# Optimization experiments

Measured on AMD Instinct MI355X. Metric: run time of the kernel, lower is better.

The kernel has to match this reference:

```python
import jax, jax.numpy as jnp
import numpy as np
from jax import lax

ALPHA = 0.3  # SSGConv alpha


def _cdist(x):
    # Euclidean distance matrix [N, N] for x: [N, H]
    n2 = jnp.sum(x * x, axis=-1)
    d2 = n2[:, None] + n2[None, :] - 2.0 * (x @ x.T)
    return jnp.sqrt(jnp.maximum(d2, 0.0))


def _prim(dist):
    # Dense O(N^2) Prim MST starting at node 0. Returns (parents, children, weights), each [N-1].
    N = dist.shape[0]
    INF = jnp.float32(1e30)
    in_tree = jnp.zeros(N, dtype=bool).at[0].set(True)
    mind = dist[0]                       # best edge weight into tree per node
    parent = jnp.zeros(N, dtype=jnp.int32)

    def step(carry, _):
        in_tree, mind, parent = carry
        d = jnp.where(in_tree, INF, mind)
        v = jnp.argmin(d).astype(jnp.int32)
        w = d[v]
        p = parent[v]
        in_tree = in_tree.at[v].set(True)
        newd = dist[v]
        upd = newd < mind
        mind = jnp.where(upd, newd, mind)
        parent = jnp.where(upd, v, parent)
        return (in_tree, mind, parent), (p, v, w)

    _, (ps, vs, ws) = lax.scan(step, (in_tree, mind, parent), None, length=N - 1)
    return ps, vs, ws


def _build_edges(features):
    # Torch code detaches edge weights via .item(); mirror with stop_gradient.
    B, N, _ = features.shape
    dist = jax.vmap(_cdist)(lax.stop_gradient(features))   # [B, N, N]
    ps, vs, ws = jax.vmap(_prim)(dist)                     # each [B, N-1]
    off = (jnp.arange(B, dtype=jnp.int32) * N)[:, None]
    a = (ps + off).ravel()
    b = (vs + off).ravel()
    src = jnp.concatenate([a, b])   # MST edges are added in both directions
    dst = jnp.concatenate([b, a])
    ew = jnp.concatenate([ws.ravel(), ws.ravel()])
    return src, dst, ew


def _gcn_norm(src, dst, ew, num_nodes):
    # PyG gcn_norm: add self loops (weight 1), symmetric deg^-1/2 normalization.
    loop = jnp.arange(num_nodes, dtype=src.dtype)
    src = jnp.concatenate([src, loop])
    dst = jnp.concatenate([dst, loop])
    ew = jnp.concatenate([ew, jnp.ones(num_nodes, ew.dtype)])
    deg = jax.ops.segment_sum(ew, dst, num_segments=num_nodes)
    dinv = jnp.where(deg > 0, lax.rsqrt(jnp.maximum(deg, 1e-30)), 0.0)
    norm = dinv[src] * ew * dinv[dst]
    return src, dst, norm


def _ssg_conv(x, src, dst, norm, W, b, num_nodes):
    # SSGConv with K=1: h = alpha*x + (1-alpha)*A_hat x, then linear.
    prop = jax.ops.segment_sum(norm[:, None] * x[src], dst, num_segments=num_nodes)
    h = ALPHA * x + (1.0 - ALPHA) * prop
    return h @ W + b


def _forward(features, W1, b1, W2, b2, W3, b3, Wd, bd, Wo, bo):
    B, N, H = features.shape
    NT = B * N
    src, dst, ew = _build_edges(features)
    src, dst, norm = _gcn_norm(src, dst, ew, NT)
    x = features.reshape(NT, H)
    x = jnp.tanh(_ssg_conv(x, src, dst, norm, W1, b1, NT))
    x = jnp.tanh(_ssg_conv(x, src, dst, norm, W2, b2, NT))
    x = jnp.tanh(_ssg_conv(x, src, dst, norm, W3, b3, NT))
    # dropout: eval mode -> identity. global_mean_pool: each graph has exactly N nodes.
    pooled = x.reshape(B, N, -1).mean(axis=1)          # [B, 2H]
    h = jnp.tanh(pooled @ Wd + bd)                     # [B, H]
    return h @ Wo + bo                                 # [B, num_labels]


def setup_inputs() -> dict:
    key = jax.random.key(0)
    ks = jax.random.split(key, 12)
    B, N, H, L = 16, 1024, 256, 8
    H2 = 2 * H

    def lin(k, fin, fout):
        s = 1.0 / np.sqrt(fin)
        k1, k2 = jax.random.split(k)
        return (jax.random.uniform(k1, (fin, fout), jnp.float32, -s, s),
                jax.random.uniform(k2, (fout,), jnp.float32, -s, s))

    W1, b1 = lin(ks[1], H, H2)
    W2, b2 = lin(ks[2], H2, H2)
    W3, b3 = lin(ks[3], H2, H2)
    Wd, bd = lin(ks[4], H2, H)
    Wo, bo = lin(ks[5], H, L)
    features = jax.random.normal(ks[0], (B, N, H), jnp.float32)
    return {"features": features, "W1": W1, "b1": b1, "W2": W2, "b2": b2,
            "W3": W3, "b3": b3, "Wd": Wd, "bd": bd, "Wo": Wo, "bo": bo}


def reference(features, W1, b1, W2, b2, W3, b3, Wd, bd, Wo, bo):
    return _forward(features, W1, b1, W2, b2, W3, b3, Wd, bd, Wo, bo)
```

## Files before the change

kernel.cpp:

```cpp
#include <hip/hip_runtime.h>
#include <math.h>

namespace {

constexpr float ALPHA = 0.3f;
constexpr int B  = 16;
constexpr int N  = 1024;
constexpr int H  = 256;
constexpr int H2 = 512;
constexpr int NT = B * N;
constexpr int NE = N - 1;
constexpr int CAP = 32;

__device__ __forceinline__ unsigned umin32(unsigned a, unsigned b) { return a < b ? a : b; }

__global__ void n2_kernel(const float* __restrict__ x, float* __restrict__ n2) {
  int wave = threadIdx.x >> 6, lane = threadIdx.x & 63;
  int row  = blockIdx.x * 4 + wave;
  float4 v = *(const float4*)(x + (size_t)row * H + lane * 4);
  float s  = v.x * v.x + v.y * v.y + v.z * v.z + v.w * v.w;
  #pragma unroll
  for (int off = 32; off; off >>= 1) s += __shfl_xor(s, off);
  if (lane == 0) n2[row] = s;
}

__global__ __launch_bounds__(256) void dist_kernel(const float* __restrict__ x,
    const float* __restrict__ n2, float* __restrict__ dist) {
  __shared__ float As[16][132], Bs[16][132];
  const int bb = blockIdx.z;
  const int i0 = blockIdx.y * 128, j0 = blockIdx.x * 128;
  const int t = threadIdx.x, tx = t & 15, ty = t >> 4;
  const float* xb = x + (size_t)bb * N * H;
  float acc[8][8] = {};
  for (int kc = 0; kc < H; kc += 16) {
    #pragma unroll
    for (int u = 0; u < 2; ++u) {
      int q = t + u * 256;
      int row = q >> 2, kf = (q & 3) * 4;
      float4 a = *(const float4*)(xb + (size_t)(i0 + row) * H + kc + kf);
      As[kf + 0][row] = a.x; As[kf + 1][row] = a.y;
      As[kf + 2][row] = a.z; As[kf + 3][row] = a.w;
      float4 bv = *(const float4*)(xb + (size_t)(j0 + row) * H + kc + kf);
      Bs[kf + 0][row] = bv.x; Bs[kf + 1][row] = bv.y;
      Bs[kf + 2][row] = bv.z; Bs[kf + 3][row] = bv.w;
    }
    __syncthreads();
    #pragma unroll
    for (int kk = 0; kk < 16; ++kk) {
      float4 a0 = *(const float4*)&As[kk][ty * 4];
      float4 a1 = *(const float4*)&As[kk][64 + ty * 4];
      float4 b0 = *(const float4*)&Bs[kk][tx * 4];
      float4 b1 = *(const float4*)&Bs[kk][64 + tx * 4];
      float ar[8] = {a0.x,a0.y,a0.z,a0.w,a1.x,a1.y,a1.z,a1.w};
      float br[8] = {b0.x,b0.y,b0.z,b0.w,b1.x,b1.y,b1.z,b1.w};
      #pragma unroll
      for (int r = 0; r < 8; ++r)
        #pragma unroll
        for (int c = 0; c < 8; ++c) acc[r][c] += ar[r] * br[c];
    }
    __syncthreads();
  }
  float n2i[8], n2j[8];
  #pragma unroll
  for (int r = 0; r < 8; ++r)
    n2i[r] = n2[bb * N + i0 + (r < 4 ? ty * 4 + r : 64 + ty * 4 + r - 4)];
  #pragma unroll
  for (int c = 0; c < 8; ++c)
    n2j[c] = n2[bb * N + j0 + (c < 4 ? tx * 4 + c : 64 + tx * 4 + c - 4)];
  #pragma unroll
  for (int r = 0; r < 8; ++r) {
    int mi = i0 + (r < 4 ? ty * 4 + r : 64 + ty * 4 + r - 4);
    float o[8];
    #pragma unroll
    for (int c = 0; c < 8; ++c) {
      float d2 = (n2i[r] + n2j[c]) - 2.0f * acc[r][c];
      o[c] = sqrtf(fmaxf(d2, 0.0f));
    }
    float* dst = dist + ((size_t)bb * N + mi) * N + j0;
    *(float4*)(dst + tx * 4)      = make_float4(o[0], o[1], o[2], o[3]);
    *(float4*)(dst + 64 + tx * 4) = make_float4(o[4], o[5], o[6], o[7]);
  }
}

__device__ __forceinline__ unsigned wave_min_u32(unsigned x) {
  unsigned t;
  t = (unsigned)__builtin_amdgcn_update_dpp((int)x, (int)x, 0x111, 0xf, 0xf, false); x = umin32(x, t);
  t = (unsigned)__builtin_amdgcn_update_dpp((int)x, (int)x, 0x112, 0xf, 0xf, false); x = umin32(x, t);
  t = (unsigned)__builtin_amdgcn_update_dpp((int)x, (int)x, 0x114, 0xf, 0xf, false); x = umin32(x, t);
  t = (unsigned)__builtin_amdgcn_update_dpp((int)x, (int)x, 0x118, 0xf, 0xf, false); x = umin32(x, t);
  x = umin32(x, (unsigned)__shfl_xor((int)x, 16));
  x = umin32(x, (unsigned)__shfl_xor((int)x, 32));
  return (unsigned)__builtin_amdgcn_readlane((int)x, 63);
}

struct Sel2 { unsigned w; int j; };

__device__ __forceinline__ Sel2 block_select(unsigned mw0, unsigned mw1,
    unsigned mw2, unsigned mw3, int wid, int lane, unsigned long long* smin) {
  unsigned lm = umin32(umin32(mw0, mw1), umin32(mw2, mw3));
  unsigned wm = wave_min_u32(lm);
  unsigned mb = (mw0 == wm ? 1u : 0u) | (mw1 == wm ? 2u : 0u) |
                (mw2 == wm ? 4u : 0u) | (mw3 == wm ? 8u : 0u);
  unsigned long long bal = __ballot(mb != 0);
  int fl = __ffsll(bal) - 1;
  int slot = __ffs((unsigned)__builtin_amdgcn_readlane((int)mb, fl)) - 1;
  int widx = (wid << 8) | (fl << 2) | slot;
  if (lane == 0)
    smin[wid] = ((unsigned long long)wm << 32) | (unsigned)widx;
  __syncthreads();
  unsigned long long k0 = smin[0], k1 = smin[1], k2 = smin[2], k3 = smin[3];
  unsigned long long ka = k0 < k1 ? k0 : k1;
  unsigned long long kb = k2 < k3 ? k2 : k3;
  unsigned long long kk = ka < kb ? ka : kb;
  __syncthreads();
  Sel2 r; r.w = (unsigned)(kk >> 32); r.j = (int)(unsigned)(kk & 0xFFFFFFFFu);
  return r;
}

__global__ __launch_bounds__(256, 1) void prim_kernel(const float* __restrict__ dist,
    int* __restrict__ ep, int* __restrict__ ev, float* __restrict__ ewt) {
  __shared__ unsigned long long smin[4];
  __shared__ int epv[NE];
  __shared__ int evv[NE];
  __shared__ float ews[NE];
  const int b = blockIdx.x;
  const int tid = threadIdx.x, wid = tid >> 6, lane = tid & 63;
  const float* Db = dist + (size_t)b * N * N;
  const int jbase = tid * 4;

  unsigned d0, d1, d2, d3;
  {
    float4 v = *(const float4*)(Db + jbase);
    d0 = __float_as_uint(v.x); d1 = __float_as_uint(v.y);
    d2 = __float_as_uint(v.z); d3 = __float_as_uint(v.w);
  }
  unsigned mw0 = d0, mw1 = d1, mw2 = d2, mw3 = d3;
  unsigned rm0 = 0, rm1 = 0, rm2 = 0, rm3 = 0;
  int pa0 = 0, pa1 = 0, pa2 = 0, pa3 = 0;
  if (tid == 0) { rm0 = ~0u; mw0 = ~0u; }

  Sel2 s0 = block_select(mw0, mw1, mw2, mw3, wid, lane, smin);
  int cj = s0.j;
  if ((cj >> 2) == tid) {
    int sl = cj & 3;
    int pv = pa0; if (sl == 1) pv = pa1; if (sl == 2) pv = pa2; if (sl == 3) pv = pa3;
    epv[0] = pv; evv[0] = cj; ews[0] = __uint_as_float(s0.w);
    if (sl == 0) { rm0 = ~0u; mw0 = ~0u; }
    if (sl == 1) { rm1 = ~0u; mw1 = ~0u; }
    if (sl == 2) { rm2 = ~0u; mw2 = ~0u; }
    if (sl == 3) { rm3 = ~0u; mw3 = ~0u; }
  }
  float4 xq = *(const float4*)(Db + (size_t)cj * N + jbase);

  for (int k = 1; k < NE; ++k) {
    unsigned r0 = __float_as_uint(xq.x), r1 = __float_as_uint(xq.y);
    unsigned r2 = __float_as_uint(xq.z), r3 = __float_as_uint(xq.w);
    unsigned q0 = r0 | rm0, q1 = r1 | rm1, q2 = r2 | rm2, q3 = r3 | rm3;
    mw0 = umin32(mw0, q0); mw1 = umin32(mw1, q1);
    mw2 = umin32(mw2, q2); mw3 = umin32(mw3, q3);
    Sel2 se = block_select(mw0, mw1, mw2, mw3, wid, lane, smin);
    const int nj = se.j;
    float4 nxt = *(const float4*)(Db + (size_t)nj * N + jbase);
    if (r0 < d0) { pa0 = cj; d0 = r0; }
    if (r1 < d1) { pa1 = cj; d1 = r1; }
    if (r2 < d2) { pa2 = cj; d2 = r2; }
    if (r3 < d3) { pa3 = cj; d3 = r3; }
    if ((nj >> 2) == tid) {
      int sl = nj & 3;
      int pv = pa0; if (sl == 1) pv = pa1; if (sl == 2) pv = pa2; if (sl == 3) pv = pa3;
      epv[k] = pv; evv[k] = nj; ews[k] = __uint_as_float(se.w);
      if (sl == 0) { rm0 = ~0u; mw0 = ~0u; }
      if (sl == 1) { rm1 = ~0u; mw1 = ~0u; }
      if (sl == 2) { rm2 = ~0u; mw2 = ~0u; }
      if (sl == 3) { rm3 = ~0u; mw3 = ~0u; }
    }
    cj = nj; xq = nxt;
  }

  __syncthreads();
  for (int e = tid; e < NE; e += 256) {
    ep[b * NE + e]  = epv[e];
    ev[b * NE + e]  = evv[e];
    ewt[b * NE + e] = ews[e];
  }
}

__global__ void adj_kernel(const int* __restrict__ ep, const int* __restrict__ ev,
    const float* __restrict__ ewt, int* __restrict__ adjI, float* __restrict__ adjW,
    int* __restrict__ cnt, float* __restrict__ dinv) {
  int i = blockIdx.x * 256 + threadIdx.x;
  int b = i >> 10, loc = i & 1023;
  const int* epb = ep + b * NE;
  const int* evb = ev + b * NE;
  const float* ewb = ewt + b * NE;
  int c = 0; float wsum = 0.0f;
  for (int k = 0; k < NE; ++k) {
    int p = epb[k], v = evb[k];
    if (p == loc || v == loc) {
      float w = ewb[k];
      wsum += w;
      int nb = (p == loc) ? v : p;
      if (c < CAP) { adjI[i * CAP + c] = (b << 10) + nb; adjW[i * CAP + c] = w; }
      ++c;
    }
  }
  cnt[i]  = c < CAP ? c : CAP;
  dinv[i] = 1.0f / sqrtf(wsum + 1.0f);
}

template <int HH>
__global__ void prop_kernel(const float* __restrict__ x, const int* __restrict__ adjI,
    const float* __restrict__ adjW, const int* __restrict__ cnt,
    const float* __restrict__ dinv, float* __restrict__ h) {
  constexpr int U = HH / 256;
  int wave = threadIdx.x >> 6, lane = threadIdx.x & 63;
  int i = blockIdx.x * 4 + wave;
  float dv = dinv[i];
  int c = cnt[i];
  float selfc = ALPHA + (1.0f - ALPHA) * dv * dv;
  float4 acc[U];
  const float* xi = x + (size_t)i * HH + lane * 4;
  #pragma unroll
  for (int u = 0; u < U; ++u) {
    float4 v = *(const float4*)(xi + u * 256);
    acc[u].x = selfc * v.x; acc[u].y = selfc * v.y;
    acc[u].z = selfc * v.z; acc[u].w = selfc * v.w;
  }
  for (int e = 0; e < c; ++e) {
    int j   = adjI[i * CAP + e];
    float w = adjW[i * CAP + e];
    float coef = (1.0f - ALPHA) * dv * (w * dinv[j]);
    const float* xj = x + (size_t)j * HH + lane * 4;
    #pragma unroll
    for (int u = 0; u < U; ++u) {
      float4 v = *(const float4*)(xj + u * 256);
      acc[u].x += coef * v.x; acc[u].y += coef * v.y;
      acc[u].z += coef * v.z; acc[u].w += coef * v.w;
    }
  }
  float* ho = h + (size_t)i * HH + lane * 4;
  #pragma unroll
  for (int u = 0; u < U; ++u) *(float4*)(ho + u * 256) = acc[u];
}

template <int K>
__global__ __launch_bounds__(256) void gemm_tanh_kernel(const float* __restrict__ A,
    const float* __restrict__ W, const float* __restrict__ bias, float* __restrict__ C) {
  __shared__ float As[16][132], Bs[16][132];
  const int m0 = blockIdx.x * 128, n0 = blockIdx.y * 128;
  const int t = threadIdx.x, tx = t & 15, ty = t >> 4;
  float acc[8][8] = {};
  for (int kc = 0; kc < K; kc += 16) {
    #pragma unroll
    for (int u = 0; u < 2; ++u) {
      int q = t + u * 256;
      int row = q >> 2, kf = (q & 3) * 4;
      float4 a = *(const float4*)(A + (size_t)(m0 + row) * K + kc + kf);
      As[kf + 0][row] = a.x; As[kf + 1][row] = a.y;
      As[kf + 2][row] = a.z; As[kf + 3][row] = a.w;
      int rowB = q >> 5, cf = (q & 31) * 4;
      *(float4*)&Bs[rowB][cf] = *(const float4*)(W + (size_t)(kc + rowB) * H2 + n0 + cf);
    }
    __syncthreads();
    #pragma unroll
    for (int kk = 0; kk < 16; ++kk) {
      float4 a0 = *(const float4*)&As[kk][ty * 4];
      float4 a1 = *(const float4*)&As[kk][64 + ty * 4];
      float4 b0 = *(const float4*)&Bs[kk][tx * 4];
      float4 b1 = *(const float4*)&Bs[kk][64 + tx * 4];
      float ar[8] = {a0.x,a0.y,a0.z,a0.w,a1.x,a1.y,a1.z,a1.w};
      float br[8] = {b0.x,b0.y,b0.z,b0.w,b1.x,b1.y,b1.z,b1.w};
      #pragma unroll
      for (int r = 0; r < 8; ++r)
        #pragma unroll
        for (int c = 0; c < 8; ++c) acc[r][c] += ar[r] * br[c];
    }
    __syncthreads();
  }
  float4 bi0 = *(const float4*)(bias + n0 + tx * 4);
  float4 bi1 = *(const float4*)(bias + n0 + 64 + tx * 4);
  float bb[8] = {bi0.x,bi0.y,bi0.z,bi0.w,bi1.x,bi1.y,bi1.z,bi1.w};
  #pragma unroll
  for (int r = 0; r < 8; ++r) {
    int m = m0 + (r < 4 ? ty * 4 + r : 64 + ty * 4 + r - 4);
    float o[8];
    #pragma unroll
    for (int c = 0; c < 8; ++c) o[c] = tanhf(acc[r][c] + bb[c]);
    float* dst = C + (size_t)m * H2 + n0;
    *(float4*)(dst + tx * 4)      = make_float4(o[0], o[1], o[2], o[3]);
    *(float4*)(dst + 64 + tx * 4) = make_float4(o[4], o[5], o[6], o[7]);
  }
}

__global__ void pool_kernel(const float* __restrict__ x, float* __restrict__ pooled) {
  int b = blockIdx.x;
  int c = blockIdx.y * 256 + threadIdx.x;
  const float* xb = x + ((size_t)b << 10) * H2 + c;
  float s = 0.0f;
  for (int i = 0; i < N; ++i) s += xb[(size_t)i * H2];
  pooled[b * H2 + c] = s * (1.0f / N);
}

__global__ void head_kernel(const float* __restrict__ pooled, const float* __restrict__ Wd,
    const float* __restrict__ bd, const float* __restrict__ Wo, const float* __restrict__ bo,
    float* __restrict__ out) {
  __shared__ float sp[512], sh[256];
  int b = blockIdx.x, t = threadIdx.x;
  sp[t] = pooled[b * H2 + t];
  sp[t + 256] = pooled[b * H2 + t + 256];
  __syncthreads();
  float acc = bd[t];
  for (int c2 = 0; c2 < 512; ++c2) acc += sp[c2] * Wd[c2 * 256 + t];
  sh[t] = tanhf(acc);
  __syncthreads();
  if (t < 8) {
    float o = bo[t];
    for (int j = 0; j < 256; ++j) o += sh[j] * Wo[j * 8 + t];
    out[b * 8 + t] = o;
  }
}

}

extern "C" void kernel_launch(void* const* d_in, const int* in_sizes, int n_in,
                              void* d_out, int out_size, void* d_ws, size_t ws_size,
                              hipStream_t stream) {
  const float* feat = (const float*)d_in[0];
  const float* W1 = (const float*)d_in[1];
  const float* b1 = (const float*)d_in[2];
  const float* W2 = (const float*)d_in[3];
  const float* b2 = (const float*)d_in[4];
  const float* W3 = (const float*)d_in[5];
  const float* b3 = (const float*)d_in[6];
  const float* Wd = (const float*)d_in[7];
  const float* bd = (const float*)d_in[8];
  const float* Wo = (const float*)d_in[9];
  const float* bo = (const float*)d_in[10];
  float* out = (float*)d_out;
  char* ws = (char*)d_ws;

  float* dist = (float*)(ws);
  float* xcur = (float*)(ws);
  float* hbuf = (float*)(ws + ((size_t)64 << 20));
  char* misc  = ws + ((size_t)96 << 20);
  int*   ep     = (int*)(misc);
  int*   ev     = (int*)(misc + 65536);
  float* ewt    = (float*)(misc + 131072);
  int*   cnt    = (int*)(misc + 196608);
  float* dinv   = (float*)(misc + 262144);
  int*   adjI   = (int*)(misc + 327680);
  float* adjW   = (float*)(misc + 327680 + 2097152);
  float* n2     = (float*)(misc + 327680 + 2 * 2097152);
  float* pooled = (float*)(misc + 327680 + 2 * 2097152 + 65536);

  n2_kernel<<<NT / 4, 256, 0, stream>>>(feat, n2);
  dist_kernel<<<dim3(8, 8, 16), 256, 0, stream>>>(feat, n2, dist);
  prim_kernel<<<B, 256, 0, stream>>>(dist, ep, ev, ewt);
  adj_kernel<<<NT / 256, 256, 0, stream>>>(ep, ev, ewt, adjI, adjW, cnt, dinv);

  prop_kernel<256><<<NT / 4, 256, 0, stream>>>(feat, adjI, adjW, cnt, dinv, hbuf);
  gemm_tanh_kernel<256><<<dim3(NT / 128, 4), 256, 0, stream>>>(hbuf, W1, b1, xcur);
  prop_kernel<512><<<NT / 4, 256, 0, stream>>>(xcur, adjI, adjW, cnt, dinv, hbuf);
  gemm_tanh_kernel<512><<<dim3(NT / 128, 4), 256, 0, stream>>>(hbuf, W2, b2, xcur);
  prop_kernel<512><<<NT / 4, 256, 0, stream>>>(xcur, adjI, adjW, cnt, dinv, hbuf);
  gemm_tanh_kernel<512><<<dim3(NT / 128, 4), 256, 0, stream>>>(hbuf, W3, b3, xcur);

  pool_kernel<<<dim3(B, H2 / 256), 256, 0, stream>>>(xcur, pooled);
  head_kernel<<<B, 256, 0, stream>>>(pooled, Wd, bd, Wo, bo, out);
}
```

Measured before the change: 1.300 ms.

## Speculatively prefetch runner-up Prim row and drop second barrier via double-buffered shared slots

```diff
diff --git a/kernel.cpp b/kernel.cpp
--- a/kernel.cpp
+++ b/kernel.cpp
@@ -93,10 +93,11 @@
   return (unsigned)__builtin_amdgcn_readlane((int)x, 63);
 }
 
-struct Sel2 { unsigned w; int j; };
-
-__device__ __forceinline__ Sel2 block_select(unsigned mw0, unsigned mw1,
-    unsigned mw2, unsigned mw3, int wid, int lane, unsigned long long* smin) {
+struct Sel3 { unsigned w; int j; int j2; };
+
+__device__ __forceinline__ Sel3 block_select2(unsigned mw0, unsigned mw1,
+    unsigned mw2, unsigned mw3, int tid, int wid, int lane,
+    unsigned long long (*s1)[4], unsigned long long (*s2)[4], int pb) {
   unsigned lm = umin32(umin32(mw0, mw1), umin32(mw2, mw3));
   unsigned wm = wave_min_u32(lm);
   unsigned mb = (mw0 == wm ? 1u : 0u) | (mw1 == wm ? 2u : 0u) |
@@ -104,22 +105,83 @@
   unsigned long long bal = __ballot(mb != 0);
   int fl = __ffsll(bal) - 1;
   int slot = __ffs((unsigned)__builtin_amdgcn_readlane((int)mb, fl)) - 1;
-  int widx = (wid << 8) | (fl << 2) | slot;
-  if (lane == 0)
-    smin[wid] = ((unsigned long long)wm << 32) | (unsigned)widx;
+  int wj = (wid << 8) | (fl << 2) | slot;
+  unsigned e0 = mw0, e1 = mw1, e2 = mw2, e3 = mw3;
+  if (tid == (wj >> 2)) {
+    int sl = wj & 3;
+    if (sl == 0) e0 = ~0u; else if (sl == 1) e1 = ~0u;
+    else if (sl == 2) e2 = ~0u; else e3 = ~0u;
+  }
+  unsigned lm2 = umin32(umin32(e0, e1), umin32(e2, e3));
+  unsigned wm2 = wave_min_u32(lm2);
+  unsigned mb2 = (e0 == wm2 ? 1u : 0u) | (e1 == wm2 ? 2u : 0u) |
+                 (e2 == wm2 ? 4u : 0u) | (e3 == wm2 ? 8u : 0u);
+  unsigned long long bal2 = __ballot(mb2 != 0);
+  int fl2 = __ffsll(bal2) - 1;
+  int slot2 = __ffs((unsigned)__builtin_amdgcn_readlane((int)mb2, fl2)) - 1;
+  int wj2 = (wid << 8) | (fl2 << 2) | slot2;
+  if (lane == 0) {
+    s1[pb][wid] = ((unsigned long long)wm  << 32) | (unsigned)wj;
+    s2[pb][wid] = ((unsigned long long)wm2 << 32) | (unsigned)wj2;
+  }
   __syncthreads();
-  unsigned long long k0 = smin[0], k1 = smin[1], k2 = smin[2], k3 = smin[3];
-  unsigned long long ka = k0 < k1 ? k0 : k1;
-  unsigned long long kb = k2 < k3 ? k2 : k3;
-  unsigned long long kk = ka < kb ? ka : kb;
-  __syncthreads();
-  Sel2 r; r.w = (unsigned)(kk >> 32); r.j = (int)(unsigned)(kk & 0xFFFFFFFFu);
+  unsigned long long a0 = s1[pb][0], a1 = s1[pb][1], a2 = s1[pb][2], a3 = s1[pb][3];
+  unsigned long long b0 = s2[pb][0], b1 = s2[pb][1], b2 = s2[pb][2], b3 = s2[pb][3];
+  unsigned long long w01 = a0 < a1 ? a0 : a1, w23 = a2 < a3 ? a2 : a3;
+  unsigned long long win = w01 < w23 ? w01 : w23;
+  unsigned long long c0 = (a0 == win) ? b0 : a0;
+  unsigned long long c1 = (a1 == win) ? b1 : a1;
+  unsigned long long c2 = (a2 == win) ? b2 : a2;
+  unsigned long long c3 = (a3 == win) ? b3 : a3;
+  unsigned long long r01 = c0 < c1 ? c0 : c1, r23 = c2 < c3 ? c2 : c3;
+  unsigned long long run = r01 < r23 ? r01 : r23;
+  Sel3 r;
+  r.w  = (unsigned)(win >> 32);
+  r.j  = (int)(unsigned)(win & 0x3FFu);
+  r.j2 = (int)(unsigned)(run & 0x3FFu);
   return r;
 }
+
+__device__ __forceinline__ void load16(const float* p, float4& x) {
+  asm volatile("global_load_dwordx4 %0, %1, off" : "=&v"(x) : "v"(p) : "memory");
+}
+
+#define PIN4(V) asm volatile("" :: "v"((V).x), "v"((V).y), "v"((V).z), "v"((V).w))
+
+#define PRIM_ITER(kk, PB, DEAD)                                                   \
+  {                                                                               \
+    asm volatile("s_waitcnt vmcnt(1)" ::: "memory");        \
+    __builtin_amdgcn_sched_barrier(0);                        \
+    PIN4(DEAD);                                       \
+    unsigned r0 = __float_as_uint(xq.x), r1 = __float_as_uint(xq.y);              \
+    unsigned r2 = __float_as_uint(xq.z), r3 = __float_as_uint(xq.w);              \
+    unsigned q0 = r0 | rm0, q1 = r1 | rm1, q2 = r2 | rm2, q3 = r3 | rm3;          \
+    mw0 = umin32(mw0, q0); mw1 = umin32(mw1, q1);                                 \
+    mw2 = umin32(mw2, q2); mw3 = umin32(mw3, q3);                                 \
+    Sel3 se = block_select2(mw0, mw1, mw2, mw3, tid, wid, lane, s1, s2, PB);      \
+    const int nj = se.j;                                                          \
+    load16(Db + (size_t)nj * N + jbase, xq);               \
+    load16(Db + (size_t)se.j2 * N + jbase, DEAD);           \
+    if (r0 < d0) { pa0 = cj; d0 = r0; }                \
+    if (r1 < d1) { pa1 = cj; d1 = r1; }                                           \
+    if (r2 < d2) { pa2 = cj; d2 = r2; }                                           \
+    if (r3 < d3) { pa3 = cj; d3 = r3; }                                           \
+    if ((nj >> 2) == tid) {                               \
+      int sl = nj & 3;                                                            \
+      int pv = pa0; if (sl == 1) pv = pa1; if (sl == 2) pv = pa2;                 \
+      if (sl == 3) pv = pa3;                                                      \
+      epv[kk] = pv; evv[kk] = nj; ews[kk] = __uint_as_float(se.w);                \
+      if (sl == 0) { rm0 = ~0u; mw0 = ~0u; }                                      \
+      if (sl == 1) { rm1 = ~0u; mw1 = ~0u; }                                      \
+      if (sl == 2) { rm2 = ~0u; mw2 = ~0u; }                                      \
+      if (sl == 3) { rm3 = ~0u; mw3 = ~0u; }                                      \
+    }                                                                             \
+    cj = nj;                                                                      \
+  }
 
 __global__ __launch_bounds__(256, 1) void prim_kernel(const float* __restrict__ dist,
     int* __restrict__ ep, int* __restrict__ ev, float* __restrict__ ewt) {
-  __shared__ unsigned long long smin[4];
+  __shared__ unsigned long long s1[2][4], s2[2][4];
   __shared__ int epv[NE];
   __shared__ int evv[NE];
   __shared__ float ews[NE];
@@ -139,7 +201,7 @@
   int pa0 = 0, pa1 = 0, pa2 = 0, pa3 = 0;
   if (tid == 0) { rm0 = ~0u; mw0 = ~0u; }
 
-  Sel2 s0 = block_select(mw0, mw1, mw2, mw3, wid, lane, smin);
+  Sel3 s0 = block_select2(mw0, mw1, mw2, mw3, tid, wid, lane, s1, s2, 0);
   int cj = s0.j;
   if ((cj >> 2) == tid) {
     int sl = cj & 3;
@@ -150,33 +212,19 @@
     if (sl == 2) { rm2 = ~0u; mw2 = ~0u; }
     if (sl == 3) { rm3 = ~0u; mw3 = ~0u; }
   }
-  float4 xq = *(const float4*)(Db + (size_t)cj * N + jbase);
-
-  for (int k = 1; k < NE; ++k) {
-    unsigned r0 = __float_as_uint(xq.x), r1 = __float_as_uint(xq.y);
-    unsigned r2 = __float_as_uint(xq.z), r3 = __float_as_uint(xq.w);
-    unsigned q0 = r0 | rm0, q1 = r1 | rm1, q2 = r2 | rm2, q3 = r3 | rm3;
-    mw0 = umin32(mw0, q0); mw1 = umin32(mw1, q1);
-    mw2 = umin32(mw2, q2); mw3 = umin32(mw3, q3);
-    Sel2 se = block_select(mw0, mw1, mw2, mw3, wid, lane, smin);
-    const int nj = se.j;
-    float4 nxt = *(const float4*)(Db + (size_t)nj * N + jbase);
-    if (r0 < d0) { pa0 = cj; d0 = r0; }
-    if (r1 < d1) { pa1 = cj; d1 = r1; }
-    if (r2 < d2) { pa2 = cj; d2 = r2; }
-    if (r3 < d3) { pa3 = cj; d3 = r3; }
-    if ((nj >> 2) == tid) {
-      int sl = nj & 3;
-      int pv = pa0; if (sl == 1) pv = pa1; if (sl == 2) pv = pa2; if (sl == 3) pv = pa3;
-      epv[k] = pv; evv[k] = nj; ews[k] = __uint_as_float(se.w);
-      if (sl == 0) { rm0 = ~0u; mw0 = ~0u; }
-      if (sl == 1) { rm1 = ~0u; mw1 = ~0u; }
-      if (sl == 2) { rm2 = ~0u; mw2 = ~0u; }
-      if (sl == 3) { rm3 = ~0u; mw3 = ~0u; }
-    }
-    cj = nj; xq = nxt;
-  }
-
+  float4 xq;
+  float4 deadA = make_float4(0.f, 0.f, 0.f, 0.f);
+  float4 deadB = make_float4(0.f, 0.f, 0.f, 0.f);
+  load16(Db + (size_t)cj * N + jbase, xq);
+  load16(Db + (size_t)s0.j2 * N + jbase, deadB);
+
+  for (int k = 1; k + 1 < NE; k += 2) {
+    PRIM_ITER(k,     1, deadA);
+    PRIM_ITER(k + 1, 0, deadB);
+  }
+
+  asm volatile("s_waitcnt vmcnt(0)" ::: "memory");
+  PIN4(deadA); PIN4(deadB); PIN4(xq);
   __syncthreads();
   for (int e = tid; e < NE; e += 256) {
     ep[b * NE + e]  = epv[e];
```

After: 1.623 ms. 24.8% more time.

## Fuse graph propagation into GEMM A-tile loading

Applied to the files above, without the earlier changes.

```diff
diff --git a/kernel.cpp b/kernel.cpp
--- a/kernel.cpp
+++ b/kernel.cpp
@@ -208,56 +208,49 @@
   dinv[i] = 1.0f / sqrtf(wsum + 1.0f);
 }
 
-template <int HH>
-__global__ void prop_kernel(const float* __restrict__ x, const int* __restrict__ adjI,
+template <int K>
+__global__ __launch_bounds__(256) void fgemm_tanh_kernel(
+    const float* __restrict__ x, const int* __restrict__ adjI,
     const float* __restrict__ adjW, const int* __restrict__ cnt,
-    const float* __restrict__ dinv, float* __restrict__ h) {
-  constexpr int U = HH / 256;
-  int wave = threadIdx.x >> 6, lane = threadIdx.x & 63;
-  int i = blockIdx.x * 4 + wave;
-  float dv = dinv[i];
-  int c = cnt[i];
-  float selfc = ALPHA + (1.0f - ALPHA) * dv * dv;
-  float4 acc[U];
-  const float* xi = x + (size_t)i * HH + lane * 4;
-  #pragma unroll
-  for (int u = 0; u < U; ++u) {
-    float4 v = *(const float4*)(xi + u * 256);
-    acc[u].x = selfc * v.x; acc[u].y = selfc * v.y;
-    acc[u].z = selfc * v.z; acc[u].w = selfc * v.w;
-  }
-  for (int e = 0; e < c; ++e) {
-    int j   = adjI[i * CAP + e];
-    float w = adjW[i * CAP + e];
-    float coef = (1.0f - ALPHA) * dv * (w * dinv[j]);
-    const float* xj = x + (size_t)j * HH + lane * 4;
-    #pragma unroll
-    for (int u = 0; u < U; ++u) {
-      float4 v = *(const float4*)(xj + u * 256);
-      acc[u].x += coef * v.x; acc[u].y += coef * v.y;
-      acc[u].z += coef * v.z; acc[u].w += coef * v.w;
-    }
-  }
-  float* ho = h + (size_t)i * HH + lane * 4;
-  #pragma unroll
-  for (int u = 0; u < U; ++u) *(float4*)(ho + u * 256) = acc[u];
-}
-
-template <int K>
-__global__ __launch_bounds__(256) void gemm_tanh_kernel(const float* __restrict__ A,
-    const float* __restrict__ W, const float* __restrict__ bias, float* __restrict__ C) {
+    const float* __restrict__ dinv, const float* __restrict__ W,
+    const float* __restrict__ bias, float* __restrict__ C) {
   __shared__ float As[16][132], Bs[16][132];
   const int m0 = blockIdx.x * 128, n0 = blockIdx.y * 128;
   const int t = threadIdx.x, tx = t & 15, ty = t >> 4;
+  const int row0 = t >> 2, kf0 = (t & 3) * 4;
+  const int row1 = row0 + 64;
+  const int ig0 = m0 + row0, ig1 = m0 + row1;
+  const float dv0 = dinv[ig0], dv1 = dinv[ig1];
+  const int   c0 = cnt[ig0],  c1 = cnt[ig1];
+  const float sf0 = ALPHA + (1.0f - ALPHA) * dv0 * dv0;
+  const float sf1 = ALPHA + (1.0f - ALPHA) * dv1 * dv1;
   float acc[8][8] = {};
   for (int kc = 0; kc < K; kc += 16) {
+    {
+      float4 a = *(const float4*)(x + (size_t)ig0 * K + kc + kf0);
+      float hx = sf0*a.x, hy = sf0*a.y, hz = sf0*a.z, hw = sf0*a.w;
+      for (int e = 0; e < c0; ++e) {
+        int j = adjI[ig0 * CAP + e];
+        float coef = (1.0f - ALPHA) * dv0 * (adjW[ig0 * CAP + e] * dinv[j]);
+        float4 v = *(const float4*)(x + (size_t)j * K + kc + kf0);
+        hx += coef*v.x; hy += coef*v.y; hz += coef*v.z; hw += coef*v.w;
+      }
+      As[kf0+0][row0]=hx; As[kf0+1][row0]=hy; As[kf0+2][row0]=hz; As[kf0+3][row0]=hw;
+    }
+    {
+      float4 a = *(const float4*)(x + (size_t)ig1 * K + kc + kf0);
+      float hx = sf1*a.x, hy = sf1*a.y, hz = sf1*a.z, hw = sf1*a.w;
+      for (int e = 0; e < c1; ++e) {
+        int j = adjI[ig1 * CAP + e];
+        float coef = (1.0f - ALPHA) * dv1 * (adjW[ig1 * CAP + e] * dinv[j]);
+        float4 v = *(const float4*)(x + (size_t)j * K + kc + kf0);
+        hx += coef*v.x; hy += coef*v.y; hz += coef*v.z; hw += coef*v.w;
+      }
+      As[kf0+0][row1]=hx; As[kf0+1][row1]=hy; As[kf0+2][row1]=hz; As[kf0+3][row1]=hw;
+    }
     #pragma unroll
     for (int u = 0; u < 2; ++u) {
       int q = t + u * 256;
-      int row = q >> 2, kf = (q & 3) * 4;
-      float4 a = *(const float4*)(A + (size_t)(m0 + row) * K + kc + kf);
-      As[kf + 0][row] = a.x; As[kf + 1][row] = a.y;
-      As[kf + 2][row] = a.z; As[kf + 3][row] = a.w;
       int rowB = q >> 5, cf = (q & 31) * 4;
       *(float4*)&Bs[rowB][cf] = *(const float4*)(W + (size_t)(kc + rowB) * H2 + n0 + cf);
     }
@@ -340,8 +333,8 @@
   char* ws = (char*)d_ws;
 
   float* dist = (float*)(ws);
-  float* xcur = (float*)(ws);
-  float* hbuf = (float*)(ws + ((size_t)64 << 20));
+  float* buf1 = (float*)(ws);
+  float* buf2 = (float*)(ws + ((size_t)64 << 20));
   char* misc  = ws + ((size_t)96 << 20);
   int*   ep     = (int*)(misc);
   int*   ev     = (int*)(misc + 65536);
@@ -358,13 +351,13 @@
   prim_kernel<<<B, 256, 0, stream>>>(dist, ep, ev, ewt);
   adj_kernel<<<NT / 256, 256, 0, stream>>>(ep, ev, ewt, adjI, adjW, cnt, dinv);
 
-  prop_kernel<256><<<NT / 4, 256, 0, stream>>>(feat, adjI, adjW, cnt, dinv, hbuf);
-  gemm_tanh_kernel<256><<<dim3(NT / 128, 4), 256, 0, stream>>>(hbuf, W1, b1, xcur);
-  prop_kernel<512><<<NT / 4, 256, 0, stream>>>(xcur, adjI, adjW, cnt, dinv, hbuf);
-  gemm_tanh_kernel<512><<<dim3(NT / 128, 4), 256, 0, stream>>>(hbuf, W2, b2, xcur);
-  prop_kernel<512><<<NT / 4, 256, 0, stream>>>(xcur, adjI, adjW, cnt, dinv, hbuf);
-  gemm_tanh_kernel<512><<<dim3(NT / 128, 4), 256, 0, stream>>>(hbuf, W3, b3, xcur);
-
-  pool_kernel<<<dim3(B, H2 / 256), 256, 0, stream>>>(xcur, pooled);
+  fgemm_tanh_kernel<256><<<dim3(NT / 128, 4), 256, 0, stream>>>(
+      feat, adjI, adjW, cnt, dinv, W1, b1, buf1);
+  fgemm_tanh_kernel<512><<<dim3(NT / 128, 4), 256, 0, stream>>>(
+      buf1, adjI, adjW, cnt, dinv, W2, b2, buf2);
+  fgemm_tanh_kernel<512><<<dim3(NT / 128, 4), 256, 0, stream>>>(
+      buf2, adjI, adjW, cnt, dinv, W3, b3, buf1);
+
+  pool_kernel<<<dim3(B, H2 / 256), 256, 0, stream>>>(buf1, pooled);
   head_kernel<<<B, 256, 0, stream>>>(pooled, Wd, bd, Wo, bo, out);
 }
```

Result: slower. 2.510 ms (+93.2%).

## Overlap layer-1 GEMM with Prim MST and exploit distance symmetry

Applied to the files above, without the earlier changes.

```diff
diff --git a/kernel.cpp b/kernel.cpp
--- a/kernel.cpp
+++ b/kernel.cpp
@@ -28,7 +28,10 @@
     const float* __restrict__ n2, float* __restrict__ dist) {
   __shared__ float As[16][132], Bs[16][132];
   const int bb = blockIdx.z;
-  const int i0 = blockIdx.y * 128, j0 = blockIdx.x * 128;
+  int idx = blockIdx.x, ti = 0;
+  while (idx >= 8 - ti) { idx -= 8 - ti; ++ti; }
+  const int tj = ti + idx;
+  const int i0 = ti * 128, j0 = tj * 128;
   const int t = threadIdx.x, tx = t & 15, ty = t >> 4;
   const float* xb = x + (size_t)bb * N * H;
   float acc[8][8] = {};
@@ -67,6 +70,8 @@
   #pragma unroll
   for (int c = 0; c < 8; ++c)
     n2j[c] = n2[bb * N + j0 + (c < 4 ? tx * 4 + c : 64 + tx * 4 + c - 4)];
+  const bool mirror = (ti != tj);
+  float* distb = dist + (size_t)bb * N * N;
   #pragma unroll
   for (int r = 0; r < 8; ++r) {
     int mi = i0 + (r < 4 ? ty * 4 + r : 64 + ty * 4 + r - 4);
@@ -76,9 +81,16 @@
       float d2 = (n2i[r] + n2j[c]) - 2.0f * acc[r][c];
       o[c] = sqrtf(fmaxf(d2, 0.0f));
     }
-    float* dst = dist + ((size_t)bb * N + mi) * N + j0;
+    float* dst = distb + (size_t)mi * N + j0;
     *(float4*)(dst + tx * 4)      = make_float4(o[0], o[1], o[2], o[3]);
     *(float4*)(dst + 64 + tx * 4) = make_float4(o[4], o[5], o[6], o[7]);
+    if (mirror) {
+      #pragma unroll
+      for (int c = 0; c < 8; ++c) {
+        int mj = j0 + (c < 4 ? tx * 4 + c : 64 + tx * 4 + c - 4);
+        distb[(size_t)mj * N + mi] = o[c];
+      }
+    }
   }
 }
 
@@ -117,71 +129,115 @@
   return r;
 }
 
-__global__ __launch_bounds__(256, 1) void prim_kernel(const float* __restrict__ dist,
-    int* __restrict__ ep, int* __restrict__ ev, float* __restrict__ ewt) {
+__global__ __launch_bounds__(256) void prim_gemm1_kernel(
+    const float* __restrict__ dist, const float* __restrict__ feat,
+    const float* __restrict__ W1, int* __restrict__ ep, int* __restrict__ ev,
+    float* __restrict__ ewt, float* __restrict__ y) {
   __shared__ unsigned long long smin[4];
   __shared__ int epv[NE];
   __shared__ int evv[NE];
   __shared__ float ews[NE];
-  const int b = blockIdx.x;
-  const int tid = threadIdx.x, wid = tid >> 6, lane = tid & 63;
-  const float* Db = dist + (size_t)b * N * N;
-  const int jbase = tid * 4;
-
-  unsigned d0, d1, d2, d3;
-  {
-    float4 v = *(const float4*)(Db + jbase);
-    d0 = __float_as_uint(v.x); d1 = __float_as_uint(v.y);
-    d2 = __float_as_uint(v.z); d3 = __float_as_uint(v.w);
-  }
-  unsigned mw0 = d0, mw1 = d1, mw2 = d2, mw3 = d3;
-  unsigned rm0 = 0, rm1 = 0, rm2 = 0, rm3 = 0;
-  int pa0 = 0, pa1 = 0, pa2 = 0, pa3 = 0;
-  if (tid == 0) { rm0 = ~0u; mw0 = ~0u; }
-
-  Sel2 s0 = block_select(mw0, mw1, mw2, mw3, wid, lane, smin);
-  int cj = s0.j;
-  if ((cj >> 2) == tid) {
-    int sl = cj & 3;
-    int pv = pa0; if (sl == 1) pv = pa1; if (sl == 2) pv = pa2; if (sl == 3) pv = pa3;
-    epv[0] = pv; evv[0] = cj; ews[0] = __uint_as_float(s0.w);
-    if (sl == 0) { rm0 = ~0u; mw0 = ~0u; }
-    if (sl == 1) { rm1 = ~0u; mw1 = ~0u; }
-    if (sl == 2) { rm2 = ~0u; mw2 = ~0u; }
-    if (sl == 3) { rm3 = ~0u; mw3 = ~0u; }
-  }
-  float4 xq = *(const float4*)(Db + (size_t)cj * N + jbase);
-
-  for (int k = 1; k < NE; ++k) {
-    unsigned r0 = __float_as_uint(xq.x), r1 = __float_as_uint(xq.y);
-    unsigned r2 = __float_as_uint(xq.z), r3 = __float_as_uint(xq.w);
-    unsigned q0 = r0 | rm0, q1 = r1 | rm1, q2 = r2 | rm2, q3 = r3 | rm3;
-    mw0 = umin32(mw0, q0); mw1 = umin32(mw1, q1);
-    mw2 = umin32(mw2, q2); mw3 = umin32(mw3, q3);
-    Sel2 se = block_select(mw0, mw1, mw2, mw3, wid, lane, smin);
-    const int nj = se.j;
-    float4 nxt = *(const float4*)(Db + (size_t)nj * N + jbase);
-    if (r0 < d0) { pa0 = cj; d0 = r0; }
-    if (r1 < d1) { pa1 = cj; d1 = r1; }
-    if (r2 < d2) { pa2 = cj; d2 = r2; }
-    if (r3 < d3) { pa3 = cj; d3 = r3; }
-    if ((nj >> 2) == tid) {
-      int sl = nj & 3;
+  __shared__ float As[16][132], Bs[16][132];
+  if (blockIdx.x < B) {
+    const int b = blockIdx.x;
+    const int tid = threadIdx.x, wid = tid >> 6, lane = tid & 63;
+    const float* Db = dist + (size_t)b * N * N;
+    const int jbase = tid * 4;
+
+    unsigned d0, d1, d2, d3;
+    {
+      float4 v = *(const float4*)(Db + jbase);
+      d0 = __float_as_uint(v.x); d1 = __float_as_uint(v.y);
+      d2 = __float_as_uint(v.z); d3 = __float_as_uint(v.w);
+    }
+    unsigned mw0 = d0, mw1 = d1, mw2 = d2, mw3 = d3;
+    unsigned rm0 = 0, rm1 = 0, rm2 = 0, rm3 = 0;
+    int pa0 = 0, pa1 = 0, pa2 = 0, pa3 = 0;
+    if (tid == 0) { rm0 = ~0u; mw0 = ~0u; }
+
+    Sel2 s0 = block_select(mw0, mw1, mw2, mw3, wid, lane, smin);
+    int cj = s0.j;
+    if ((cj >> 2) == tid) {
+      int sl = cj & 3;
       int pv = pa0; if (sl == 1) pv = pa1; if (sl == 2) pv = pa2; if (sl == 3) pv = pa3;
-      epv[k] = pv; evv[k] = nj; ews[k] = __uint_as_float(se.w);
+      epv[0] = pv; evv[0] = cj; ews[0] = __uint_as_float(s0.w);
       if (sl == 0) { rm0 = ~0u; mw0 = ~0u; }
       if (sl == 1) { rm1 = ~0u; mw1 = ~0u; }
       if (sl == 2) { rm2 = ~0u; mw2 = ~0u; }
       if (sl == 3) { rm3 = ~0u; mw3 = ~0u; }
     }
-    cj = nj; xq = nxt;
-  }
-
-  __syncthreads();
-  for (int e = tid; e < NE; e += 256) {
-    ep[b * NE + e]  = epv[e];
-    ev[b * NE + e]  = evv[e];
-    ewt[b * NE + e] = ews[e];
+    float4 xq = *(const float4*)(Db + (size_t)cj * N + jbase);
+
+    for (int k = 1; k < NE; ++k) {
+      unsigned r0 = __float_as_uint(xq.x), r1 = __float_as_uint(xq.y);
+      unsigned r2 = __float_as_uint(xq.z), r3 = __float_as_uint(xq.w);
+      unsigned q0 = r0 | rm0, q1 = r1 | rm1, q2 = r2 | rm2, q3 = r3 | rm3;
+      mw0 = umin32(mw0, q0); mw1 = umin32(mw1, q1);
+      mw2 = umin32(mw2, q2); mw3 = umin32(mw3, q3);
+      Sel2 se = block_select(mw0, mw1, mw2, mw3, wid, lane, smin);
+      const int nj = se.j;
+      float4 nxt = *(const float4*)(Db + (size_t)nj * N + jbase);
+      if (r0 < d0) { pa0 = cj; d0 = r0; }
+      if (r1 < d1) { pa1 = cj; d1 = r1; }
+      if (r2 < d2) { pa2 = cj; d2 = r2; }
+      if (r3 < d3) { pa3 = cj; d3 = r3; }
+      if ((nj >> 2) == tid) {
+        int sl = nj & 3;
+        int pv = pa0; if (sl == 1) pv = pa1; if (sl == 2) pv = pa2; if (sl == 3) pv = pa3;
+        epv[k] = pv; evv[k] = nj; ews[k] = __uint_as_float(se.w);
+        if (sl == 0) { rm0 = ~0u; mw0 = ~0u; }
+        if (sl == 1) { rm1 = ~0u; mw1 = ~0u; }
+        if (sl == 2) { rm2 = ~0u; mw2 = ~0u; }
+        if (sl == 3) { rm3 = ~0u; mw3 = ~0u; }
+      }
+      cj = nj; xq = nxt;
+    }
+
+    __syncthreads();
+    for (int e = tid; e < NE; e += 256) {
+      ep[b * NE + e]  = epv[e];
+      ev[b * NE + e]  = evv[e];
+      ewt[b * NE + e] = ews[e];
+    }
+  } else {
+    const int gb = blockIdx.x - B;
+    const int m0 = (gb >> 2) * 128, n0 = (gb & 3) * 128;
+    const int t = threadIdx.x, tx = t & 15, ty = t >> 4;
+    float acc[8][8] = {};
+    for (int kc = 0; kc < H; kc += 16) {
+      #pragma unroll
+      for (int u = 0; u < 2; ++u) {
+        int q = t + u * 256;
+        int row = q >> 2, kf = (q & 3) * 4;
+        float4 a = *(const float4*)(feat + (size_t)(m0 + row) * H + kc + kf);
+        As[kf + 0][row] = a.x; As[kf + 1][row] = a.y;
+        As[kf + 2][row] = a.z; As[kf + 3][row] = a.w;
+        int rowB = q >> 5, cf = (q & 31) * 4;
+        *(float4*)&Bs[rowB][cf] = *(const float4*)(W1 + (size_t)(kc + rowB) * H2 + n0 + cf);
+      }
+      __syncthreads();
+      #pragma unroll
+      for (int kk = 0; kk < 16; ++kk) {
+        float4 a0 = *(const float4*)&As[kk][ty * 4];
+        float4 a1 = *(const float4*)&As[kk][64 + ty * 4];
+        float4 b0 = *(const float4*)&Bs[kk][tx * 4];
+        float4 b1 = *(const float4*)&Bs[kk][64 + tx * 4];
+        float ar[8] = {a0.x,a0.y,a0.z,a0.w,a1.x,a1.y,a1.z,a1.w};
+        float br[8] = {b0.x,b0.y,b0.z,b0.w,b1.x,b1.y,b1.z,b1.w};
+        #pragma unroll
+        for (int r = 0; r < 8; ++r)
+          #pragma unroll
+          for (int c = 0; c < 8; ++c) acc[r][c] += ar[r] * br[c];
+      }
+      __syncthreads();
+    }
+    #pragma unroll
+    for (int r = 0; r < 8; ++r) {
+      int m = m0 + (r < 4 ? ty * 4 + r : 64 + ty * 4 + r - 4);
+      float* dst = y + (size_t)m * H2 + n0;
+      *(float4*)(dst + tx * 4)      = make_float4(acc[r][0], acc[r][1], acc[r][2], acc[r][3]);
+      *(float4*)(dst + 64 + tx * 4) = make_float4(acc[r][4], acc[r][5], acc[r][6], acc[r][7]);
+    }
   }
 }
 
@@ -208,6 +264,46 @@
   dinv[i] = 1.0f / sqrtf(wsum + 1.0f);
 }
 
+__global__ void finish1_kernel(const float* __restrict__ y, const int* __restrict__ adjI,
+    const float* __restrict__ adjW, const int* __restrict__ cnt,
+    const float* __restrict__ dinv, const float* __restrict__ b1,
+    float* __restrict__ out1) {
+  int wave = threadIdx.x >> 6, lane = threadIdx.x & 63;
+  int i = blockIdx.x * 4 + wave;
+  float dv = dinv[i];
+  int c = cnt[i];
+  float selfc = ALPHA + (1.0f - ALPHA) * dv * dv;
+  float4 acc[2];
+  const float* yi = y + (size_t)i * H2 + lane * 4;
+  #pragma unroll
+  for (int u = 0; u < 2; ++u) {
+    float4 v = *(const float4*)(yi + u * 256);
+    acc[u].x = selfc * v.x; acc[u].y = selfc * v.y;
+    acc[u].z = selfc * v.z; acc[u].w = selfc * v.w;
+  }
+  for (int e = 0; e < c; ++e) {
+    int j   = adjI[i * CAP + e];
+    float w = adjW[i * CAP + e];
+    float coef = (1.0f - ALPHA) * dv * (w * dinv[j]);
+    const float* yj = y + (size_t)j * H2 + lane * 4;
+    #pragma unroll
+    for (int u = 0; u < 2; ++u) {
+      float4 v = *(const float4*)(yj + u * 256);
+      acc[u].x += coef * v.x; acc[u].y += coef * v.y;
+      acc[u].z += coef * v.z; acc[u].w += coef * v.w;
+    }
+  }
+  float* ho = out1 + (size_t)i * H2 + lane * 4;
+  #pragma unroll
+  for (int u = 0; u < 2; ++u) {
+    float4 bb = *(const float4*)(b1 + lane * 4 + u * 256);
+    float4 o;
+    o.x = tanhf(acc[u].x + bb.x); o.y = tanhf(acc[u].y + bb.y);
+    o.z = tanhf(acc[u].z + bb.z); o.w = tanhf(acc[u].w + bb.w);
+    *(float4*)(ho + u * 256) = o;
+  }
+}
+
 template <int HH>
 __global__ void prop_kernel(const float* __restrict__ x, const int* __restrict__ adjI,
     const float* __restrict__ adjW, const int* __restrict__ cnt,
@@ -340,7 +436,10 @@
   char* ws = (char*)d_ws;
 
   float* dist = (float*)(ws);
-  float* xcur = (float*)(ws);
+  float* out1 = (float*)(ws);
+  float* x2   = (float*)(ws + ((size_t)32 << 20));
+  float* x3   = (float*)(ws);
+  float* ybuf = (float*)(ws + ((size_t)64 << 20));
   float* hbuf = (float*)(ws + ((size_t)64 << 20));
   char* misc  = ws + ((size_t)96 << 20);
   int*   ep     = (int*)(misc);
@@ -354,17 +453,17 @@
   float* pooled = (float*)(misc + 327680 + 2 * 2097152 + 65536);
 
   n2_kernel<<<NT / 4, 256, 0, stream>>>(feat, n2);
-  dist_kernel<<<dim3(8, 8, 16), 256, 0, stream>>>(feat, n2, dist);
-  prim_kernel<<<B, 256, 0, stream>>>(dist, ep, ev, ewt);
+  dist_kernel<<<dim3(36, 1, 16), 256, 0, stream>>>(feat, n2, dist);
+  prim_gemm1_kernel<<<B + (NT / 128) * 4, 256, 0, stream>>>(
+      dist, feat, W1, ep, ev, ewt, ybuf);
   adj_kernel<<<NT / 256, 256, 0, stream>>>(ep, ev, ewt, adjI, adjW, cnt, dinv);
 
-  prop_kernel<256><<<NT / 4, 256, 0, stream>>>(feat, adjI, adjW, cnt, dinv, hbuf);
-  gemm_tanh_kernel<256><<<dim3(NT / 128, 4), 256, 0, stream>>>(hbuf, W1, b1, xcur);
-  prop_kernel<512><<<NT / 4, 256, 0, stream>>>(xcur, adjI, adjW, cnt, dinv, hbuf);
-  gemm_tanh_kernel<512><<<dim3(NT / 128, 4), 256, 0, stream>>>(hbuf, W2, b2, xcur);
-  prop_kernel<512><<<NT / 4, 256, 0, stream>>>(xcur, adjI, adjW, cnt, dinv, hbuf);
-  gemm_tanh_kernel<512><<<dim3(NT / 128, 4), 256, 0, stream>>>(hbuf, W3, b3, xcur);
-
-  pool_kernel<<<dim3(B, H2 / 256), 256, 0, stream>>>(xcur, pooled);
+  finish1_kernel<<<NT / 4, 256, 0, stream>>>(ybuf, adjI, adjW, cnt, dinv, b1, out1);
+  prop_kernel<512><<<NT / 4, 256, 0, stream>>>(out1, adjI, adjW, cnt, dinv, hbuf);
+  gemm_tanh_kernel<512><<<dim3(NT / 128, 4), 256, 0, stream>>>(hbuf, W2, b2, x2);
+  prop_kernel<512><<<NT / 4, 256, 0, stream>>>(x2, adjI, adjW, cnt, dinv, hbuf);
+  gemm_tanh_kernel<512><<<dim3(NT / 128, 4), 256, 0, stream>>>(hbuf, W3, b3, x3);
+
+  pool_kernel<<<dim3(B, H2 / 256), 256, 0, stream>>>(x3, pooled);
   head_kernel<<<B, 256, 0, stream>>>(pooled, Wd, bd, Wo, bo, out);
 }
```

Measured after the change: 1.228 ms. 1.06x faster.
